# Kernel tuning notes

Hardware: AMD Instinct MI355X
Metric: run time of the kernel (lower is better)

The kernel has to match this reference:

```python
import jax, jax.numpy as jnp
import numpy as np


def setup_inputs() -> dict:
    key = jax.random.key(0)
    k1, k2 = jax.random.split(key)
    C, H, W = 64, 1024, 1024
    NUM_SP = 2048
    x = jax.random.normal(k1, (C, H, W), dtype=jnp.float32)
    sp = jax.random.randint(k2, (H, W), 0, NUM_SP, dtype=jnp.int32)
    return {"x": x, "sp": sp, "num_segments": NUM_SP}


def reference(x, sp, num_segments):
    # x: [C, H, W], sp: [H, W] superpixel labels in [0, num_segments)
    C, H, W = x.shape
    N = H * W
    sp_flat = sp.reshape(N)                      # [N]
    x_flat = x.reshape(C, N).T                   # [N, C]
    # Per-superpixel, per-channel sums and pixel counts (single-pass segment reduce)
    sums = jax.ops.segment_sum(x_flat, sp_flat, num_segments=num_segments)   # [S, C]
    counts = jax.ops.segment_sum(jnp.ones((N,), dtype=x.dtype), sp_flat,
                                 num_segments=num_segments)                  # [S]
    means = sums / jnp.maximum(counts, 1.0)[:, None]                         # [S, C]
    # Broadcast each superpixel's mean back to its pixels
    out = means[sp_flat].T.reshape(C, H, W)
    return out
```

## Files before the change

### kernel.cpp

```cpp
#include <hip/hip_runtime.h>

#define NUM_SP 2048
#define CG 4
#define NG_SUM 11
#define SUM_THREADS 1024
#define SUM_CHUNKS 46
#define BCAST_THREADS 512
#define BCAST_CHUNKS 64
#define FBITS 21
#define FMASK ((1ULL << FBITS) - 1ULL)


__global__ __launch_bounds__(256) void zero_kernel(float* ws, int n) {
    int i = blockIdx.x * 256 + threadIdx.x;
    int stride = gridDim.x * 256;
    for (; i < n; i += stride) ws[i] = 0.0f;
}

__global__ __launch_bounds__(256) void count_kernel(const int* __restrict__ sp,
                                                    float* __restrict__ counts, int N) {
    __shared__ int hist[NUM_SP];
    for (int i = threadIdx.x; i < NUM_SP; i += 256) hist[i] = 0;
    __syncthreads();
    int per = (N + gridDim.x - 1) / gridDim.x;
    int base = blockIdx.x * per;
    int end = base + per; if (end > N) end = N;
    for (int p = base + threadIdx.x; p < end; p += 256) {
        atomicAdd(&hist[sp[p]], 1);
    }
    __syncthreads();
    for (int i = threadIdx.x; i < NUM_SP; i += 256) {
        int c = hist[i];
        if (c) atomicAdd(&counts[i], (float)c);
    }
}

template <int CHN>
__device__ __forceinline__ void sum_body(const float* __restrict__ xg,
                                         const int* __restrict__ sp,
                                         unsigned long long* __restrict__ acc,
                                         int base, int end, int N,
                                         float scale, float bsr) {
    int p = base + (int)threadIdx.x;
    for (; p + SUM_THREADS < end; p += 2 * SUM_THREADS) {
        int p2 = p + SUM_THREADS;
        int s0 = sp[p];
        int s1 = sp[p2];
        float a[CHN], b[CHN];
#pragma unroll
        for (int c = 0; c < CHN; ++c) { a[c] = xg[c * N + p]; b[c] = xg[c * N + p2]; }
        unsigned long long q00 = 0, q01 = 0, q10 = 0, q11 = 0;
#pragma unroll
        for (int c = 0; c < CHN; ++c) {
            unsigned long long ua = (unsigned int)fmaf(a[c], scale, bsr);
            unsigned long long ub = (unsigned int)fmaf(b[c], scale, bsr);
            int sh = (c % 3) * FBITS;
            if (c < 3) { q00 |= ua << sh; q10 |= ub << sh; }
            else       { q01 |= ua << sh; q11 |= ub << sh; }
        }
        atomicAdd(&acc[(s0 << 1) + 0], q00);
        if (CHN > 3) atomicAdd(&acc[(s0 << 1) + 1], q01);
        atomicAdd(&acc[(s1 << 1) + 0], q10);
        if (CHN > 3) atomicAdd(&acc[(s1 << 1) + 1], q11);
    }
    for (; p < end; p += SUM_THREADS) {
        int s = sp[p];
        unsigned long long q0 = 0, q1 = 0;
#pragma unroll
        for (int c = 0; c < CHN; ++c) {
            unsigned long long u = (unsigned int)fmaf(xg[c * N + p], scale, bsr);
            int sh = (c % 3) * FBITS;
            if (c < 3) q0 |= u << sh; else q1 |= u << sh;
        }
        atomicAdd(&acc[(s << 1) + 0], q0);
        if (CHN > 3) atomicAdd(&acc[(s << 1) + 1], q1);
    }
}

__global__ __launch_bounds__(SUM_THREADS, 8) void sum_kernel(
        const float* __restrict__ x, const int* __restrict__ sp,
        unsigned long long* __restrict__ outq,
        int N, int chunks, int use_partials, float scale, float bsr) {
    __shared__ unsigned long long acc[NUM_SP * 2];
    for (int i = threadIdx.x; i < NUM_SP * 2; i += SUM_THREADS) acc[i] = 0ULL;
    __syncthreads();

    const int gs = blockIdx.y;
    const int chunk = blockIdx.x;
    const int per = (N + chunks - 1) / chunks;
    const int base = chunk * per;
    int end = base + per; if (end > N) end = N;
    const float* xg = x + (size_t)gs * 6 * N;

    if (gs == NG_SUM - 1) sum_body<4>(xg, sp, acc, base, end, N, scale, bsr);
    else                  sum_body<6>(xg, sp, acc, base, end, N, scale, bsr);
    __syncthreads();

    unsigned long long* dst = outq + (size_t)(use_partials ? (chunk * NG_SUM + gs) : gs)
                                     * (NUM_SP * 2);
    for (int i = threadIdx.x; i < NUM_SP * 2; i += SUM_THREADS) {
        unsigned long long v = acc[i];
        if (use_partials) dst[i] = v;
        else if (v) atomicAdd(&dst[i], v);
    }
}

__global__ __launch_bounds__(256) void mean_kernel(const unsigned long long* __restrict__ partq,
                                                   const float* __restrict__ counts,
                                                   float* __restrict__ means_gm,
                                                   int SC, int chunks, float scale) {
    int i = blockIdx.x * 256 + threadIdx.x;
    if (i >= SC) return;
    int s = i & (NUM_SP - 1);
    int c = i >> 11;
    int gs = c / 6;
    int f = c - gs * 6;
    int j = f / 3, sub = f - j * 3;
    unsigned long long fs = 0;
    for (int k = 0; k < chunks; ++k) {
        unsigned long long q = partq[(size_t)(k * NG_SUM + gs) * (NUM_SP * 2) + (s << 1) + j];
        fs += (q >> (sub * FBITS)) & FMASK;
    }
    float cnt = counts[s];
    double sv = ((double)fs - (double)cnt * (double)(6.0f * scale)) / (double)scale;
    means_gm[((size_t)(c >> 2) * NUM_SP + s) * 4 + (c & 3)] = (float)(sv / fmax((double)cnt, 1.0));
}

__global__ __launch_bounds__(BCAST_THREADS, 8) void bcast_kernel(
        const int* __restrict__ sp, const float4* __restrict__ means_gm4,
        float* __restrict__ out, int N) {
    __shared__ float4 tbl[NUM_SP];
    const int g = blockIdx.y;
    for (int e = threadIdx.x; e < NUM_SP; e += BCAST_THREADS)
        tbl[e] = means_gm4[(size_t)g * NUM_SP + e];
    __syncthreads();

    const int per = (N + gridDim.x - 1) / gridDim.x;
    const int base = blockIdx.x * per;
    int end = base + per; if (end > N) end = N;
    float* o0 = out + (size_t)(g * CG + 0) * N;
    float* o1 = out + (size_t)(g * CG + 1) * N;
    float* o2 = out + (size_t)(g * CG + 2) * N;
    float* o3 = out + (size_t)(g * CG + 3) * N;

    int p = base + (int)threadIdx.x;
    for (; p + BCAST_THREADS < end; p += 2 * BCAST_THREADS) {
        int p2 = p + BCAST_THREADS;
        int s0 = sp[p];
        int s1 = sp[p2];
        float4 m0 = tbl[s0];
        float4 m1 = tbl[s1];
        o0[p] = m0.x; o1[p] = m0.y; o2[p] = m0.z; o3[p] = m0.w;
        o0[p2] = m1.x; o1[p2] = m1.y; o2[p2] = m1.z; o3[p2] = m1.w;
    }
    for (; p < end; p += BCAST_THREADS) {
        float4 m = tbl[sp[p]];
        o0[p] = m.x; o1[p] = m.y; o2[p] = m.z; o3[p] = m.w;
    }
}

extern "C" void kernel_launch(void* const* d_in, const int* in_sizes, int n_in,
                              void* d_out, int out_size, void* d_ws, size_t ws_size,
                              hipStream_t stream) {
    const float* x = (const float*)d_in[0];
    const int* sp = (const int*)d_in[1];
    const int N = in_sizes[1];
    const int C = in_sizes[0] / N;
    float* out = (float*)d_out;
    float* ws = (float*)d_ws;

    const int S = NUM_SP;
    const int SC = S * C;
    const int NG = C / CG;

    float* counts = ws;
    float* means = ws + S;
    unsigned long long* partq = (unsigned long long*)(ws + S + SC);

    const size_t part_floats_per_chunk = (size_t)NG_SUM * NUM_SP * 2 * 2;
    size_t ws_floats = ws_size / sizeof(float);
    size_t avail = (ws_floats > (size_t)(S + SC)) ? ws_floats - (size_t)(S + SC) : 0;
    int chunks = (int)(avail / part_floats_per_chunk);
    if (chunks > SUM_CHUNKS) chunks = SUM_CHUNKS;
    int use_partials = (chunks >= 32) ? 1 : 0;
    int grid_chunks = use_partials ? chunks : SUM_CHUNKS;
    float scale = use_partials ? 2048.0f : 128.0f;
    float bsr = 6.0f * scale + 0.5f;

    zero_kernel<<<64, 256, 0, stream>>>(ws, use_partials ? S
                                            : S + SC + (int)part_floats_per_chunk);
    count_kernel<<<256, 256, 0, stream>>>(sp, counts, N);
    dim3 g2(grid_chunks, NG_SUM);
    sum_kernel<<<g2, SUM_THREADS, 0, stream>>>(x, sp, partq, N, grid_chunks,
                                               use_partials, scale, bsr);
    mean_kernel<<<(SC + 255) / 256, 256, 0, stream>>>(partq, counts, means, SC,
                                                      use_partials ? grid_chunks : 1, scale);
    dim3 gb(BCAST_CHUNKS, NG);
    bcast_kernel<<<gb, BCAST_THREADS, 0, stream>>>(sp, (const float4*)means, out, N);
}
```

Measured before the change: 494.8 us.

## Fold pixel counts into sum kernel and vectorize broadcast over 8 channels

Drops the separate count kernel and instead packs a per-pixel count bit field into the spare high bits of the last channel group's second atomic word. A small kernel then extracts the counts from the partials. The broadcast kernel now handles 8 channels per block, reads labels as int4 and writes float4, which cuts the label re-reads and makes the stores wide. The sum loop loses its 2x manual unroll, and occupancy hints for the broadcast kernel drop to 4 blocks per SM, since its shared table doubles.

```diff
diff --git a/kernel.cpp b/kernel.cpp
--- a/kernel.cpp
+++ b/kernel.cpp
@@ -1,14 +1,15 @@
 #include <hip/hip_runtime.h>
 
 #define NUM_SP 2048
-#define CG 4
 #define NG_SUM 11
 #define SUM_THREADS 1024
 #define SUM_CHUNKS 46
 #define BCAST_THREADS 512
 #define BCAST_CHUNKS 64
+#define NGB 8
 #define FBITS 21
 #define FMASK ((1ULL << FBITS) - 1ULL)
+#define CNT_SHIFT 42
 
 
 __global__ __launch_bounds__(256) void zero_kernel(float* ws, int n) {
@@ -17,63 +18,27 @@
     for (; i < n; i += stride) ws[i] = 0.0f;
 }
 
-__global__ __launch_bounds__(256) void count_kernel(const int* __restrict__ sp,
-                                                    float* __restrict__ counts, int N) {
-    __shared__ int hist[NUM_SP];
-    for (int i = threadIdx.x; i < NUM_SP; i += 256) hist[i] = 0;
-    __syncthreads();
-    int per = (N + gridDim.x - 1) / gridDim.x;
-    int base = blockIdx.x * per;
-    int end = base + per; if (end > N) end = N;
-    for (int p = base + threadIdx.x; p < end; p += 256) {
-        atomicAdd(&hist[sp[p]], 1);
-    }
-    __syncthreads();
-    for (int i = threadIdx.x; i < NUM_SP; i += 256) {
-        int c = hist[i];
-        if (c) atomicAdd(&counts[i], (float)c);
-    }
-}
-
-template <int CHN>
+template <int CHN, bool WCNT>
 __device__ __forceinline__ void sum_body(const float* __restrict__ xg,
                                          const int* __restrict__ sp,
                                          unsigned long long* __restrict__ acc,
                                          int base, int end, int N,
                                          float scale, float bsr) {
-    int p = base + (int)threadIdx.x;
-    for (; p + SUM_THREADS < end; p += 2 * SUM_THREADS) {
-        int p2 = p + SUM_THREADS;
-        int s0 = sp[p];
-        int s1 = sp[p2];
-        float a[CHN], b[CHN];
+    for (int p = base + (int)threadIdx.x; p < end; p += SUM_THREADS) {
+        int s = sp[p];
+        float v[CHN];
 #pragma unroll
-        for (int c = 0; c < CHN; ++c) { a[c] = xg[c * N + p]; b[c] = xg[c * N + p2]; }
-        unsigned long long q00 = 0, q01 = 0, q10 = 0, q11 = 0;
-#pragma unroll
-        for (int c = 0; c < CHN; ++c) {
-            unsigned long long ua = (unsigned int)fmaf(a[c], scale, bsr);
-            unsigned long long ub = (unsigned int)fmaf(b[c], scale, bsr);
-            int sh = (c % 3) * FBITS;
-            if (c < 3) { q00 |= ua << sh; q10 |= ub << sh; }
-            else       { q01 |= ua << sh; q11 |= ub << sh; }
-        }
-        atomicAdd(&acc[(s0 << 1) + 0], q00);
-        if (CHN > 3) atomicAdd(&acc[(s0 << 1) + 1], q01);
-        atomicAdd(&acc[(s1 << 1) + 0], q10);
-        if (CHN > 3) atomicAdd(&acc[(s1 << 1) + 1], q11);
-    }
-    for (; p < end; p += SUM_THREADS) {
-        int s = sp[p];
+        for (int c = 0; c < CHN; ++c) v[c] = xg[c * N + p];
         unsigned long long q0 = 0, q1 = 0;
 #pragma unroll
         for (int c = 0; c < CHN; ++c) {
-            unsigned long long u = (unsigned int)fmaf(xg[c * N + p], scale, bsr);
-            int sh = (c % 3) * FBITS;
-            if (c < 3) q0 |= u << sh; else q1 |= u << sh;
+            unsigned long long u = (unsigned int)fmaf(v[c], scale, bsr);
+            if (c < 3) q0 |= u << (c * FBITS);
+            else       q1 |= u << ((c - 3) * FBITS);
         }
+        if (WCNT) q1 |= (1ULL << CNT_SHIFT);
         atomicAdd(&acc[(s << 1) + 0], q0);
-        if (CHN > 3) atomicAdd(&acc[(s << 1) + 1], q1);
+        atomicAdd(&acc[(s << 1) + 1], q1);
     }
 }
 
@@ -92,8 +57,8 @@
     int end = base + per; if (end > N) end = N;
     const float* xg = x + (size_t)gs * 6 * N;
 
-    if (gs == NG_SUM - 1) sum_body<4>(xg, sp, acc, base, end, N, scale, bsr);
-    else                  sum_body<6>(xg, sp, acc, base, end, N, scale, bsr);
+    if (gs == NG_SUM - 1) sum_body<4, true >(xg, sp, acc, base, end, N, scale, bsr);
+    else                  sum_body<6, false>(xg, sp, acc, base, end, N, scale, bsr);
     __syncthreads();
 
     unsigned long long* dst = outq + (size_t)(use_partials ? (chunk * NG_SUM + gs) : gs)
@@ -105,9 +70,20 @@
     }
 }
 
+__global__ __launch_bounds__(256) void cnt_kernel(const unsigned long long* __restrict__ partq,
+                                                  float* __restrict__ counts, int chunks) {
+    int s = blockIdx.x * 256 + threadIdx.x;
+    if (s >= NUM_SP) return;
+    unsigned long long c = 0;
+    for (int k = 0; k < chunks; ++k)
+        c += partq[(size_t)(k * NG_SUM + (NG_SUM - 1)) * (NUM_SP * 2) + (s << 1) + 1]
+             >> CNT_SHIFT;
+    counts[s] = (float)c;
+}
+
 __global__ __launch_bounds__(256) void mean_kernel(const unsigned long long* __restrict__ partq,
                                                    const float* __restrict__ counts,
-                                                   float* __restrict__ means_gm,
+                                                   float* __restrict__ means,
                                                    int SC, int chunks, float scale) {
     int i = blockIdx.x * 256 + threadIdx.x;
     if (i >= SC) return;
@@ -123,39 +99,61 @@
     }
     float cnt = counts[s];
     double sv = ((double)fs - (double)cnt * (double)(6.0f * scale)) / (double)scale;
-    means_gm[((size_t)(c >> 2) * NUM_SP + s) * 4 + (c & 3)] = (float)(sv / fmax((double)cnt, 1.0));
+    means[((size_t)(c >> 3) * NUM_SP + s) * 8 + (c & 7)] = (float)(sv / fmax((double)cnt, 1.0));
 }
 
-__global__ __launch_bounds__(BCAST_THREADS, 8) void bcast_kernel(
-        const int* __restrict__ sp, const float4* __restrict__ means_gm4,
+__global__ __launch_bounds__(BCAST_THREADS, 4) void bcast_kernel(
+        const int* __restrict__ sp, const float4* __restrict__ means4,
         float* __restrict__ out, int N) {
-    __shared__ float4 tbl[NUM_SP];
+    __shared__ float4 tbl[NUM_SP * 2];
     const int g = blockIdx.y;
-    for (int e = threadIdx.x; e < NUM_SP; e += BCAST_THREADS)
-        tbl[e] = means_gm4[(size_t)g * NUM_SP + e];
+    for (int e = threadIdx.x; e < NUM_SP * 2; e += BCAST_THREADS)
+        tbl[e] = means4[(size_t)g * (NUM_SP * 2) + e];
     __syncthreads();
 
-    const int per = (N + gridDim.x - 1) / gridDim.x;
+    int per = (N + gridDim.x - 1) / gridDim.x;
+    per = (per + 3) & ~3;
     const int base = blockIdx.x * per;
     int end = base + per; if (end > N) end = N;
-    float* o0 = out + (size_t)(g * CG + 0) * N;
-    float* o1 = out + (size_t)(g * CG + 1) * N;
-    float* o2 = out + (size_t)(g * CG + 2) * N;
-    float* o3 = out + (size_t)(g * CG + 3) * N;
+    if (end <= base) return;
+    const int end4 = base + ((end - base) & ~3);
 
-    int p = base + (int)threadIdx.x;
-    for (; p + BCAST_THREADS < end; p += 2 * BCAST_THREADS) {
-        int p2 = p + BCAST_THREADS;
-        int s0 = sp[p];
-        int s1 = sp[p2];
-        float4 m0 = tbl[s0];
-        float4 m1 = tbl[s1];
-        o0[p] = m0.x; o1[p] = m0.y; o2[p] = m0.z; o3[p] = m0.w;
-        o0[p2] = m1.x; o1[p2] = m1.y; o2[p2] = m1.z; o3[p2] = m1.w;
+    const int4* sp4 = (const int4*)sp;
+    float4* o0 = (float4*)(out + (size_t)(g * NGB + 0) * N);
+    float4* o1 = (float4*)(out + (size_t)(g * NGB + 1) * N);
+    float4* o2 = (float4*)(out + (size_t)(g * NGB + 2) * N);
+    float4* o3 = (float4*)(out + (size_t)(g * NGB + 3) * N);
+    float4* o4 = (float4*)(out + (size_t)(g * NGB + 4) * N);
+    float4* o5 = (float4*)(out + (size_t)(g * NGB + 5) * N);
+    float4* o6 = (float4*)(out + (size_t)(g * NGB + 6) * N);
+    float4* o7 = (float4*)(out + (size_t)(g * NGB + 7) * N);
+
+    for (int q = (base >> 2) + (int)threadIdx.x; q < (end4 >> 2); q += BCAST_THREADS) {
+        int4 s4 = sp4[q];
+        float4 ax = tbl[(s4.x << 1)], ay = tbl[(s4.x << 1) + 1];
+        float4 bx = tbl[(s4.y << 1)], by = tbl[(s4.y << 1) + 1];
+        float4 cx = tbl[(s4.z << 1)], cy = tbl[(s4.z << 1) + 1];
+        float4 dx = tbl[(s4.w << 1)], dy = tbl[(s4.w << 1) + 1];
+        o0[q] = make_float4(ax.x, bx.x, cx.x, dx.x);
+        o1[q] = make_float4(ax.y, bx.y, cx.y, dx.y);
+        o2[q] = make_float4(ax.z, bx.z, cx.z, dx.z);
+        o3[q] = make_float4(ax.w, bx.w, cx.w, dx.w);
+        o4[q] = make_float4(ay.x, by.x, cy.x, dy.x);
+        o5[q] = make_float4(ay.y, by.y, cy.y, dy.y);
+        o6[q] = make_float4(ay.z, by.z, cy.z, dy.z);
+        o7[q] = make_float4(ay.w, by.w, cy.w, dy.w);
     }
-    for (; p < end; p += BCAST_THREADS) {
-        float4 m = tbl[sp[p]];
-        o0[p] = m.x; o1[p] = m.y; o2[p] = m.z; o3[p] = m.w;
+    for (int p = end4 + (int)threadIdx.x; p < end; p += BCAST_THREADS) {
+        int s = sp[p];
+        float4 t0 = tbl[(s << 1)], t1 = tbl[(s << 1) + 1];
+        out[(size_t)(g * NGB + 0) * N + p] = t0.x;
+        out[(size_t)(g * NGB + 1) * N + p] = t0.y;
+        out[(size_t)(g * NGB + 2) * N + p] = t0.z;
+        out[(size_t)(g * NGB + 3) * N + p] = t0.w;
+        out[(size_t)(g * NGB + 4) * N + p] = t1.x;
+        out[(size_t)(g * NGB + 5) * N + p] = t1.y;
+        out[(size_t)(g * NGB + 6) * N + p] = t1.z;
+        out[(size_t)(g * NGB + 7) * N + p] = t1.w;
     }
 }
 
@@ -171,7 +169,6 @@
 
     const int S = NUM_SP;
     const int SC = S * C;
-    const int NG = C / CG;
 
     float* counts = ws;
     float* means = ws + S;
@@ -187,14 +184,16 @@
     float scale = use_partials ? 2048.0f : 128.0f;
     float bsr = 6.0f * scale + 0.5f;
 
-    zero_kernel<<<64, 256, 0, stream>>>(ws, use_partials ? S
-                                            : S + SC + (int)part_floats_per_chunk);
-    count_kernel<<<256, 256, 0, stream>>>(sp, counts, N);
+    if (!use_partials) {
+        zero_kernel<<<64, 256, 0, stream>>>((float*)partq, (int)part_floats_per_chunk);
+    }
     dim3 g2(grid_chunks, NG_SUM);
     sum_kernel<<<g2, SUM_THREADS, 0, stream>>>(x, sp, partq, N, grid_chunks,
                                                use_partials, scale, bsr);
+    int rchunks = use_partials ? grid_chunks : 1;
+    cnt_kernel<<<NUM_SP / 256, 256, 0, stream>>>(partq, counts, rchunks);
     mean_kernel<<<(SC + 255) / 256, 256, 0, stream>>>(partq, counts, means, SC,
-                                                      use_partials ? grid_chunks : 1, scale);
-    dim3 gb(BCAST_CHUNKS, NG);
+                                                      rchunks, scale);
+    dim3 gb(BCAST_CHUNKS, NGB);
     bcast_kernel<<<gb, BCAST_THREADS, 0, stream>>>(sp, (const float4*)means, out, N);
 }
```

Result: no change. 495.0 us (+0.0%).
